# Performance work log

Measured on AMD Instinct MI355X. Metric: run time of the kernel, lower is better.

Reference implementation:

```python
import jax, jax.numpy as jnp
import numpy as np

N_NODES = 100000
N_EDGES = 1600000
IN_C, HID_C, OUT_C = 128, 64, 32


def gcn_conv(x, src, dst, dinv, W, b):
    # GCNConv: h = x W; out[i] = sum_{j->i} norm_ji * h[j] + b
    h = x @ W                                   # [N, C_out]
    norm = dinv[src] * dinv[dst]                # [E_tot]
    msg = h[src] * norm[:, None]                # gather + scale
    out = jax.ops.segment_sum(msg, dst, num_segments=N_NODES)
    return out + b


def setup_inputs() -> dict:
    key = jax.random.key(0)
    k1, k2, k3, k4 = jax.random.split(key, 4)
    x = jax.random.normal(k1, (N_NODES, IN_C), dtype=jnp.float32)
    edge_index = jax.random.randint(k2, (2, N_EDGES), 0, N_NODES, dtype=jnp.int64)
    # Glorot-ish init for weights
    W1 = jax.random.normal(k3, (IN_C, HID_C), dtype=jnp.float32) * (1.0 / np.sqrt(IN_C))
    b1 = jnp.zeros((HID_C,), dtype=jnp.float32)
    W2 = jax.random.normal(k4, (HID_C, OUT_C), dtype=jnp.float32) * (1.0 / np.sqrt(HID_C))
    b2 = jnp.zeros((OUT_C,), dtype=jnp.float32)
    return {"x": x, "edge_index": edge_index, "W1": W1, "b1": b1, "W2": W2, "b2": b2}


def reference(x, edge_index, W1, b1, W2, b2):
    # Add self loops (GCNConv default), compute symmetric normalization once.
    loop = jnp.arange(N_NODES, dtype=edge_index.dtype)
    src = jnp.concatenate([edge_index[0], loop])   # [E + N]
    dst = jnp.concatenate([edge_index[1], loop])
    deg = jax.ops.segment_sum(jnp.ones_like(src, dtype=x.dtype), dst,
                              num_segments=N_NODES)
    dinv = jnp.where(deg > 0, jax.lax.rsqrt(jnp.maximum(deg, 1e-12)), 0.0)

    h = gcn_conv(x, src, dst, dinv, W1, b1)
    h = jax.nn.relu(h)
    # F.dropout with training=False (eval mode) is identity
    out = gcn_conv(h, src, dst, dinv, W2, b2)
    return out
```

## Files before the change

kernel.cpp:

```cpp
#include <hip/hip_runtime.h>

#define N_NODES 100000
#define N_EDGES 1600000
#define IN_C 128
#define HID_C 64
#define OUT_C 32

#define NBUCK 782
#define NBLK_B 256
#define CHUNK 6250
#define BSTRIDE 1024
#define MAXPT 12

#define GROWS 16
#define GEMM_BLKS 6250

typedef unsigned int uint;
typedef unsigned short ushort;

__device__ inline ushort f2bf(float f) {
    uint u = __float_as_uint(f);
    u += 0x7fff + ((u >> 16) & 1);
    return (ushort)(u >> 16);
}
__device__ inline float bf2f(ushort h) {
    return __uint_as_float(((uint)h) << 16);
}


__global__ __launch_bounds__(256) void k_bucket_count(const int* __restrict__ dst,
                                                      int* __restrict__ bcnt) {
    __shared__ int h[NBUCK];
    int t = threadIdx.x;
    for (int b = t; b < NBUCK; b += 256) h[b] = 0;
    __syncthreads();
    int base = blockIdx.x * CHUNK;
    int end = base + CHUNK;
    for (int i = base + t; i < end; i += 256) atomicAdd(&h[dst[i] >> 7], 1);
    __syncthreads();
    for (int b = t; b < NBUCK; b += 256) bcnt[blockIdx.x * BSTRIDE + b] = h[b];
}


__global__ __launch_bounds__(256) void k_col_scan(const int* __restrict__ bcnt,
                                                  int* __restrict__ off,
                                                  int* __restrict__ total) {
    __shared__ int ps[256];
    int t = threadIdx.x, b = blockIdx.x;
    int l = bcnt[t * BSTRIDE + b];
    ps[t] = l;
    __syncthreads();
    for (int o = 1; o < 256; o <<= 1) {
        int u = (t >= o) ? ps[t - o] : 0;
        __syncthreads();
        ps[t] += u;
        __syncthreads();
    }
    off[t * BSTRIDE + b] = ps[t] - l;
    if (t == 255) total[b] = ps[255];
}


__global__ __launch_bounds__(256) void k_bucket_scan(const int* __restrict__ total,
                                                     int* __restrict__ bucket_start,
                                                     int* __restrict__ row_start) {
    __shared__ int ps[256];
    int t = threadIdx.x;
    int v[4];
    int base = t * 4;
#pragma unroll
    for (int q = 0; q < 4; ++q) v[q] = (base + q < NBUCK) ? total[base + q] : 0;
    ps[t] = v[0] + v[1] + v[2] + v[3];
    __syncthreads();
    for (int o = 1; o < 256; o <<= 1) {
        int u = (t >= o) ? ps[t - o] : 0;
        __syncthreads();
        ps[t] += u;
        __syncthreads();
    }
    int run = (t > 0) ? ps[t - 1] : 0;
#pragma unroll
    for (int q = 0; q < 4; ++q) {
        if (base + q <= NBUCK) bucket_start[base + q] = run;
        run += v[q];
    }
    if (t == 0) row_start[N_NODES] = N_EDGES;
}


__global__ __launch_bounds__(256) void k_scatter_fat(const int* __restrict__ src,
                                                     const int* __restrict__ dst,
                                                     const int* __restrict__ bucket_start,
                                                     const int* __restrict__ off,
                                                     int* __restrict__ tmp,
                                                     const float* __restrict__ x,
                                                     const float* __restrict__ W1,
                                                     ushort* __restrict__ h1b) {
    __shared__ float smem[GROWS * IN_C];
    int t = threadIdx.x;
    if (blockIdx.x < NBLK_B) {
        int* cur = (int*)smem;
        for (int b = t; b < NBUCK; b += 256)
            cur[b] = bucket_start[b] + off[blockIdx.x * BSTRIDE + b];
        __syncthreads();
        int base = blockIdx.x * CHUNK;
        int end = base + CHUNK;
        for (int i = base + t; i < end; i += 256) {
            int s = src[i], d = dst[i];
            int b = d >> 7;
            int p = atomicAdd(&cur[b], 1);
            tmp[p] = (s << 7) | (d & 127);
        }
    } else {
        int rowbase = (blockIdx.x - NBLK_B) * GROWS;
#pragma unroll
        for (int q = 0; q < 8; ++q)
            smem[q * 256 + t] = x[rowbase * IN_C + q * 256 + t];
        __syncthreads();
        int wave = t >> 6, lane = t & 63;
        int rl0 = wave * 4;
        float a0 = 0.f, a1 = 0.f, a2 = 0.f, a3 = 0.f;
#pragma unroll 8
        for (int k = 0; k < IN_C; ++k) {
            float w = W1[k * HID_C + lane];
            a0 += smem[(rl0 + 0) * IN_C + k] * w;
            a1 += smem[(rl0 + 1) * IN_C + k] * w;
            a2 += smem[(rl0 + 2) * IN_C + k] * w;
            a3 += smem[(rl0 + 3) * IN_C + k] * w;
        }
        int row = rowbase + rl0;
        h1b[(row + 0) * HID_C + lane] = f2bf(a0);
        h1b[(row + 1) * HID_C + lane] = f2bf(a1);
        h1b[(row + 2) * HID_C + lane] = f2bf(a2);
        h1b[(row + 3) * HID_C + lane] = f2bf(a3);
    }
}


__global__ __launch_bounds__(256) void k_csr_build(const int* __restrict__ bucket_start,
                                                   const int* __restrict__ tmp,
                                                   int* __restrict__ row_start,
                                                   int* __restrict__ eidx,
                                                   float* __restrict__ dinv) {
    __shared__ int h[128];
    __shared__ int cur[128];
    int b = blockIdx.x, t = threadIdx.x;
    int e0 = bucket_start[b], e1 = bucket_start[b + 1];
    if (t < 128) h[t] = 0;
    int pk[MAXPT];
#pragma unroll
    for (int k = 0; k < MAXPT; ++k) {
        int i = e0 + k * 256 + t;
        pk[k] = (i < e1) ? tmp[i] : -1;
    }
    __syncthreads();
#pragma unroll
    for (int k = 0; k < MAXPT; ++k)
        if (pk[k] >= 0) atomicAdd(&h[pk[k] & 127], 1);
    for (int i = e0 + MAXPT * 256 + t; i < e1; i += 256)
        atomicAdd(&h[tmp[i] & 127], 1);
    __syncthreads();
    int d0 = (t < 128) ? h[t] : 0;
    for (int o = 1; o < 128; o <<= 1) {
        int u = (t >= o && t < 128) ? h[t - o] : 0;
        __syncthreads();
        if (t < 128) h[t] += u;
        __syncthreads();
    }
    int g = b * 128 + t;
    if (t < 128 && g < N_NODES) {
        int ex = h[t] - d0;
        row_start[g] = e0 + ex;
        cur[t]       = e0 + ex;
        dinv[g] = rsqrtf((float)(d0 + 1));
    }
    __syncthreads();
#pragma unroll
    for (int k = 0; k < MAXPT; ++k)
        if (pk[k] >= 0) {
            int p = atomicAdd(&cur[pk[k] & 127], 1);
            eidx[p] = pk[k] >> 7;
        }
    for (int i = e0 + MAXPT * 256 + t; i < e1; i += 256) {
        int v = tmp[i];
        int p = atomicAdd(&cur[v & 127], 1);
        eidx[p] = v >> 7;
    }
}


__global__ __launch_bounds__(256) void k_gather1f(const int* __restrict__ row_start,
                                                  const int* __restrict__ eidx,
                                                  const uint* __restrict__ h1u,
                                                  const float* __restrict__ dinv,
                                                  const float* __restrict__ b1,
                                                  const float* __restrict__ W2,
                                                  ushort* __restrict__ hs2b) {
    __shared__ float a1s[8][HID_C];
    __shared__ float W2s[HID_C * OUT_C];
    int t = threadIdx.x;
    for (int i = t; i < HID_C * OUT_C; i += 256) W2s[i] = W2[i];
    int sub = t & 31;
    int r = t >> 5;
    float2 bb = *(const float2*)&b1[sub * 2];

    for (int g = 0; g < 4; ++g) {
        int node = (blockIdx.x * 4 + g) * 8 + r;
        float dn = dinv[node];
        int rs = row_start[node];
        int re = row_start[node + 1];
        uint su = h1u[node * 32 + sub];
        float accx = dn * __uint_as_float(su << 16);
        float accy = dn * __uint_as_float(su & 0xffff0000u);
        int j = rs;
        for (; j + 7 < re; j += 8) {
            int s0 = eidx[j],     s1 = eidx[j + 1], s2 = eidx[j + 2], s3 = eidx[j + 3];
            int s4 = eidx[j + 4], s5 = eidx[j + 5], s6 = eidx[j + 6], s7 = eidx[j + 7];
            float g0 = dinv[s0], g1 = dinv[s1], g2 = dinv[s2], g3 = dinv[s3];
            float g4 = dinv[s4], g5 = dinv[s5], g6 = dinv[s6], g7 = dinv[s7];
            uint u0 = h1u[s0 * 32 + sub], u1 = h1u[s1 * 32 + sub];
            uint u2 = h1u[s2 * 32 + sub], u3 = h1u[s3 * 32 + sub];
            uint u4 = h1u[s4 * 32 + sub], u5 = h1u[s5 * 32 + sub];
            uint u6 = h1u[s6 * 32 + sub], u7 = h1u[s7 * 32 + sub];
            accx += g0 * __uint_as_float(u0 << 16) + g1 * __uint_as_float(u1 << 16)
                  + g2 * __uint_as_float(u2 << 16) + g3 * __uint_as_float(u3 << 16)
                  + g4 * __uint_as_float(u4 << 16) + g5 * __uint_as_float(u5 << 16)
                  + g6 * __uint_as_float(u6 << 16) + g7 * __uint_as_float(u7 << 16);
            accy += g0 * __uint_as_float(u0 & 0xffff0000u) + g1 * __uint_as_float(u1 & 0xffff0000u)
                  + g2 * __uint_as_float(u2 & 0xffff0000u) + g3 * __uint_as_float(u3 & 0xffff0000u)
                  + g4 * __uint_as_float(u4 & 0xffff0000u) + g5 * __uint_as_float(u5 & 0xffff0000u)
                  + g6 * __uint_as_float(u6 & 0xffff0000u) + g7 * __uint_as_float(u7 & 0xffff0000u);
        }
        for (; j + 3 < re; j += 4) {
            int s0 = eidx[j], s1 = eidx[j + 1], s2 = eidx[j + 2], s3 = eidx[j + 3];
            float g0 = dinv[s0], g1 = dinv[s1], g2 = dinv[s2], g3 = dinv[s3];
            uint u0 = h1u[s0 * 32 + sub], u1 = h1u[s1 * 32 + sub];
            uint u2 = h1u[s2 * 32 + sub], u3 = h1u[s3 * 32 + sub];
            accx += g0 * __uint_as_float(u0 << 16) + g1 * __uint_as_float(u1 << 16)
                  + g2 * __uint_as_float(u2 << 16) + g3 * __uint_as_float(u3 << 16);
            accy += g0 * __uint_as_float(u0 & 0xffff0000u) + g1 * __uint_as_float(u1 & 0xffff0000u)
                  + g2 * __uint_as_float(u2 & 0xffff0000u) + g3 * __uint_as_float(u3 & 0xffff0000u);
        }
        for (; j < re; ++j) {
            int s = eidx[j];
            float gg = dinv[s];
            uint u = h1u[s * 32 + sub];
            accx += gg * __uint_as_float(u << 16);
            accy += gg * __uint_as_float(u & 0xffff0000u);
        }
        __syncthreads();
        a1s[r][sub * 2 + 0] = fmaxf(dn * accx + bb.x, 0.f);
        a1s[r][sub * 2 + 1] = fmaxf(dn * accy + bb.y, 0.f);
        __syncthreads();

        float sum = 0.f;
#pragma unroll 8
        for (int k = 0; k < HID_C; ++k)
            sum += a1s[r][k] * W2s[k * OUT_C + sub];
        hs2b[node * OUT_C + sub] = f2bf(dn * sum);
    }
}


__global__ __launch_bounds__(256) void k_gather2(const int* __restrict__ row_start,
                                                 const int* __restrict__ eidx,
                                                 const ushort* __restrict__ hs2b,
                                                 const float* __restrict__ dinv,
                                                 const float* __restrict__ b2,
                                                 float* __restrict__ out) {
    int t = threadIdx.x;
    int sub = t & 31;
    int node = blockIdx.x * 8 + (t >> 5);

    float dn = dinv[node];
    int rs = row_start[node];
    int re = row_start[node + 1];
    float acc = bf2f(hs2b[node * OUT_C + sub]);
    int j = rs;
    for (; j + 7 < re; j += 8) {
        int s0 = eidx[j],     s1 = eidx[j + 1], s2 = eidx[j + 2], s3 = eidx[j + 3];
        int s4 = eidx[j + 4], s5 = eidx[j + 5], s6 = eidx[j + 6], s7 = eidx[j + 7];
        float v0 = bf2f(hs2b[s0 * OUT_C + sub]);
        float v1 = bf2f(hs2b[s1 * OUT_C + sub]);
        float v2 = bf2f(hs2b[s2 * OUT_C + sub]);
        float v3 = bf2f(hs2b[s3 * OUT_C + sub]);
        float v4 = bf2f(hs2b[s4 * OUT_C + sub]);
        float v5 = bf2f(hs2b[s5 * OUT_C + sub]);
        float v6 = bf2f(hs2b[s6 * OUT_C + sub]);
        float v7 = bf2f(hs2b[s7 * OUT_C + sub]);
        acc += ((v0 + v1) + (v2 + v3)) + ((v4 + v5) + (v6 + v7));
    }
    for (; j + 3 < re; j += 4) {
        int s0 = eidx[j], s1 = eidx[j + 1], s2 = eidx[j + 2], s3 = eidx[j + 3];
        float v0 = bf2f(hs2b[s0 * OUT_C + sub]);
        float v1 = bf2f(hs2b[s1 * OUT_C + sub]);
        float v2 = bf2f(hs2b[s2 * OUT_C + sub]);
        float v3 = bf2f(hs2b[s3 * OUT_C + sub]);
        acc += (v0 + v1) + (v2 + v3);
    }
    for (; j < re; ++j) acc += bf2f(hs2b[eidx[j] * OUT_C + sub]);

    out[node * OUT_C + sub] = dn * acc + b2[sub];
}

extern "C" void kernel_launch(void* const* d_in, const int* in_sizes, int n_in,
                              void* d_out, int out_size, void* d_ws, size_t ws_size,
                              hipStream_t stream) {
    const float* x  = (const float*)d_in[0];
    const int* ei   = (const int*)d_in[1];
    const float* W1 = (const float*)d_in[2];
    const float* b1 = (const float*)d_in[3];
    const float* W2 = (const float*)d_in[4];
    const float* b2 = (const float*)d_in[5];
    float* out = (float*)d_out;

    const int* src = ei;
    const int* dst = ei + N_EDGES;

    char* ws = (char*)d_ws;
    int*    row_start    = (int*)(ws + 0);
    float*  dinv         = (float*)(ws + 400128);
    int*    bucket_start = (int*)(ws + 800256);
    int*    total        = (int*)(ws + 804352);
    int*    bcnt         = (int*)(ws + 808448);
    int*    off          = (int*)(ws + 1857024);
    int*    eidx         = (int*)(ws + 2905600);
    int*    tmp          = (int*)(ws + 9305600);
    ushort* h1b          = (ushort*)(ws + 15705600);
    ushort* hs2b         = (ushort*)(ws + 28505600);

    k_bucket_count<<<NBLK_B, 256, 0, stream>>>(dst, bcnt);
    k_col_scan<<<NBUCK, 256, 0, stream>>>(bcnt, off, total);
    k_bucket_scan<<<1, 256, 0, stream>>>(total, bucket_start, row_start);

    k_scatter_fat<<<NBLK_B + GEMM_BLKS, 256, 0, stream>>>(src, dst, bucket_start, off,
                                                          tmp, x, W1, h1b);
    k_csr_build<<<NBUCK, 256, 0, stream>>>(bucket_start, tmp, row_start, eidx, dinv);

    k_gather1f<<<N_NODES / 32, 256, 0, stream>>>(row_start, eidx, (const uint*)h1b,
                                                 dinv, b1, W2, hs2b);
    k_gather2<<<N_NODES / 8, 256, 0, stream>>>(row_start, eidx, hs2b, dinv, b2, out);
}
```

Baseline: 162.6 us.

## Use bf16 MFMA for first GEMM and prescale h1 by dinv in CSR build

```diff
diff --git a/kernel.cpp b/kernel.cpp
--- a/kernel.cpp
+++ b/kernel.cpp
@@ -12,11 +12,12 @@
 #define BSTRIDE 1024
 #define MAXPT 12
 
-#define GROWS 16
-#define GEMM_BLKS 6250
+#define MF_BLKS 1563
 
 typedef unsigned int uint;
 typedef unsigned short ushort;
+typedef __attribute__((ext_vector_type(8))) short bf16x8;
+typedef __attribute__((ext_vector_type(4))) float f32x4;
 
 __device__ inline ushort f2bf(float f) {
     uint u = __float_as_uint(f);
@@ -96,10 +97,10 @@
                                                      const float* __restrict__ x,
                                                      const float* __restrict__ W1,
                                                      ushort* __restrict__ h1b) {
-    __shared__ float smem[GROWS * IN_C];
+    __shared__ uint smu[4096];
     int t = threadIdx.x;
     if (blockIdx.x < NBLK_B) {
-        int* cur = (int*)smem;
+        int* cur = (int*)smu;
         for (int b = t; b < NBUCK; b += 256)
             cur[b] = bucket_start[b] + off[blockIdx.x * BSTRIDE + b];
         __syncthreads();
@@ -112,27 +113,58 @@
             tmp[p] = (s << 7) | (d & 127);
         }
     } else {
-        int rowbase = (blockIdx.x - NBLK_B) * GROWS;
-#pragma unroll
-        for (int q = 0; q < 8; ++q)
-            smem[q * 256 + t] = x[rowbase * IN_C + q * 256 + t];
+        int g = blockIdx.x - NBLK_B;
+#pragma unroll
+        for (int i = 0; i < 16; ++i) {
+            int lin = i * 256 + t;
+            int frag = lin >> 8;
+            int lane_ = (lin >> 2) & 63;
+            int dw = lin & 3;
+            int k = ((frag >> 2) << 5) + ((lane_ >> 4) << 3) + dw * 2;
+            int c = ((frag & 3) << 4) + (lane_ & 15);
+            smu[lin] = ((uint)f2bf(W1[(k + 1) * HID_C + c]) << 16) | f2bf(W1[k * HID_C + c]);
+        }
         __syncthreads();
         int wave = t >> 6, lane = t & 63;
-        int rl0 = wave * 4;
-        float a0 = 0.f, a1 = 0.f, a2 = 0.f, a3 = 0.f;
-#pragma unroll 8
-        for (int k = 0; k < IN_C; ++k) {
-            float w = W1[k * HID_C + lane];
-            a0 += smem[(rl0 + 0) * IN_C + k] * w;
-            a1 += smem[(rl0 + 1) * IN_C + k] * w;
-            a2 += smem[(rl0 + 2) * IN_C + k] * w;
-            a3 += smem[(rl0 + 3) * IN_C + k] * w;
-        }
-        int row = rowbase + rl0;
-        h1b[(row + 0) * HID_C + lane] = f2bf(a0);
-        h1b[(row + 1) * HID_C + lane] = f2bf(a1);
-        h1b[(row + 2) * HID_C + lane] = f2bf(a2);
-        h1b[(row + 3) * HID_C + lane] = f2bf(a3);
+        int row0 = g * 64 + wave * 16;
+        bf16x8 bfr[4][4];
+#pragma unroll
+        for (int kt = 0; kt < 4; ++kt)
+#pragma unroll
+            for (int ct = 0; ct < 4; ++ct)
+                bfr[kt][ct] = *(bf16x8*)&smu[((kt * 4 + ct) * 64 + lane) * 4];
+        int arow = row0 + (lane & 15);
+        if (arow > N_NODES - 1) arow = N_NODES - 1;
+        int kbase = (lane >> 4) * 8;
+        f32x4 acc0 = {0.f, 0.f, 0.f, 0.f}, acc1 = {0.f, 0.f, 0.f, 0.f};
+        f32x4 acc2 = {0.f, 0.f, 0.f, 0.f}, acc3 = {0.f, 0.f, 0.f, 0.f};
+#pragma unroll
+        for (int kt = 0; kt < 4; ++kt) {
+            const float* xp = &x[arow * IN_C + kt * 32 + kbase];
+            float4 u0 = *(const float4*)xp;
+            float4 u1 = *(const float4*)(xp + 4);
+            union { uint u[4]; bf16x8 v; } A;
+            A.u[0] = ((uint)f2bf(u0.y) << 16) | f2bf(u0.x);
+            A.u[1] = ((uint)f2bf(u0.w) << 16) | f2bf(u0.z);
+            A.u[2] = ((uint)f2bf(u1.y) << 16) | f2bf(u1.x);
+            A.u[3] = ((uint)f2bf(u1.w) << 16) | f2bf(u1.z);
+            acc0 = __builtin_amdgcn_mfma_f32_16x16x32_bf16(A.v, bfr[kt][0], acc0, 0, 0, 0);
+            acc1 = __builtin_amdgcn_mfma_f32_16x16x32_bf16(A.v, bfr[kt][1], acc1, 0, 0, 0);
+            acc2 = __builtin_amdgcn_mfma_f32_16x16x32_bf16(A.v, bfr[kt][2], acc2, 0, 0, 0);
+            acc3 = __builtin_amdgcn_mfma_f32_16x16x32_bf16(A.v, bfr[kt][3], acc3, 0, 0, 0);
+        }
+        int rbase = row0 + ((lane >> 4) << 2);
+        int cb = lane & 15;
+#pragma unroll
+        for (int r = 0; r < 4; ++r) {
+            int row = rbase + r;
+            if (row < N_NODES) {
+                h1b[row * HID_C + cb]      = f2bf(acc0[r]);
+                h1b[row * HID_C + 16 + cb] = f2bf(acc1[r]);
+                h1b[row * HID_C + 32 + cb] = f2bf(acc2[r]);
+                h1b[row * HID_C + 48 + cb] = f2bf(acc3[r]);
+            }
+        }
     }
 }
 
@@ -141,9 +173,11 @@
                                                    const int* __restrict__ tmp,
                                                    int* __restrict__ row_start,
                                                    int* __restrict__ eidx,
-                                                   float* __restrict__ dinv) {
+                                                   float* __restrict__ dinv,
+                                                   uint* __restrict__ h1u) {
     __shared__ int h[128];
     __shared__ int cur[128];
+    __shared__ float dl[128];
     int b = blockIdx.x, t = threadIdx.x;
     int e0 = bucket_start[b], e1 = bucket_start[b + 1];
     if (t < 128) h[t] = 0;
@@ -172,7 +206,9 @@
         int ex = h[t] - d0;
         row_start[g] = e0 + ex;
         cur[t]       = e0 + ex;
-        dinv[g] = rsqrtf((float)(d0 + 1));
+        float dv = rsqrtf((float)(d0 + 1));
+        dinv[g] = dv;
+        dl[t] = dv;
     }
     __syncthreads();
 #pragma unroll
@@ -185,6 +221,18 @@
         int v = tmp[i];
         int p = atomicAdd(&cur[v & 127], 1);
         eidx[p] = v >> 7;
+    }
+    int bu = b * 128 * (HID_C / 2);
+    for (int i = t; i < 128 * (HID_C / 2); i += 256) {
+        int rl = i >> 5;
+        int gg = b * 128 + rl;
+        if (gg < N_NODES) {
+            float dv = dl[rl];
+            uint v = h1u[bu + i];
+            float lo = __uint_as_float(v << 16) * dv;
+            float hi = __uint_as_float(v & 0xffff0000u) * dv;
+            h1u[bu + i] = ((uint)f2bf(hi) << 16) | f2bf(lo);
+        }
     }
 }
 
@@ -210,43 +258,38 @@
         int rs = row_start[node];
         int re = row_start[node + 1];
         uint su = h1u[node * 32 + sub];
-        float accx = dn * __uint_as_float(su << 16);
-        float accy = dn * __uint_as_float(su & 0xffff0000u);
+        float accx = __uint_as_float(su << 16);
+        float accy = __uint_as_float(su & 0xffff0000u);
         int j = rs;
         for (; j + 7 < re; j += 8) {
             int s0 = eidx[j],     s1 = eidx[j + 1], s2 = eidx[j + 2], s3 = eidx[j + 3];
             int s4 = eidx[j + 4], s5 = eidx[j + 5], s6 = eidx[j + 6], s7 = eidx[j + 7];
-            float g0 = dinv[s0], g1 = dinv[s1], g2 = dinv[s2], g3 = dinv[s3];
-            float g4 = dinv[s4], g5 = dinv[s5], g6 = dinv[s6], g7 = dinv[s7];
             uint u0 = h1u[s0 * 32 + sub], u1 = h1u[s1 * 32 + sub];
             uint u2 = h1u[s2 * 32 + sub], u3 = h1u[s3 * 32 + sub];
             uint u4 = h1u[s4 * 32 + sub], u5 = h1u[s5 * 32 + sub];
             uint u6 = h1u[s6 * 32 + sub], u7 = h1u[s7 * 32 + sub];
-            accx += g0 * __uint_as_float(u0 << 16) + g1 * __uint_as_float(u1 << 16)
-                  + g2 * __uint_as_float(u2 << 16) + g3 * __uint_as_float(u3 << 16)
-                  + g4 * __uint_as_float(u4 << 16) + g5 * __uint_as_float(u5 << 16)
-                  + g6 * __uint_as_float(u6 << 16) + g7 * __uint_as_float(u7 << 16);
-            accy += g0 * __uint_as_float(u0 & 0xffff0000u) + g1 * __uint_as_float(u1 & 0xffff0000u)
-                  + g2 * __uint_as_float(u2 & 0xffff0000u) + g3 * __uint_as_float(u3 & 0xffff0000u)
-                  + g4 * __uint_as_float(u4 & 0xffff0000u) + g5 * __uint_as_float(u5 & 0xffff0000u)
-                  + g6 * __uint_as_float(u6 & 0xffff0000u) + g7 * __uint_as_float(u7 & 0xffff0000u);
+            accx += (__uint_as_float(u0 << 16) + __uint_as_float(u1 << 16))
+                  + (__uint_as_float(u2 << 16) + __uint_as_float(u3 << 16))
+                  + (__uint_as_float(u4 << 16) + __uint_as_float(u5 << 16))
+                  + (__uint_as_float(u6 << 16) + __uint_as_float(u7 << 16));
+            accy += (__uint_as_float(u0 & 0xffff0000u) + __uint_as_float(u1 & 0xffff0000u))
+                  + (__uint_as_float(u2 & 0xffff0000u) + __uint_as_float(u3 & 0xffff0000u))
+                  + (__uint_as_float(u4 & 0xffff0000u) + __uint_as_float(u5 & 0xffff0000u))
+                  + (__uint_as_float(u6 & 0xffff0000u) + __uint_as_float(u7 & 0xffff0000u));
         }
         for (; j + 3 < re; j += 4) {
             int s0 = eidx[j], s1 = eidx[j + 1], s2 = eidx[j + 2], s3 = eidx[j + 3];
-            float g0 = dinv[s0], g1 = dinv[s1], g2 = dinv[s2], g3 = dinv[s3];
             uint u0 = h1u[s0 * 32 + sub], u1 = h1u[s1 * 32 + sub];
             uint u2 = h1u[s2 * 32 + sub], u3 = h1u[s3 * 32 + sub];
-            accx += g0 * __uint_as_float(u0 << 16) + g1 * __uint_as_float(u1 << 16)
-                  + g2 * __uint_as_float(u2 << 16) + g3 * __uint_as_float(u3 << 16);
-            accy += g0 * __uint_as_float(u0 & 0xffff0000u) + g1 * __uint_as_float(u1 & 0xffff0000u)
-                  + g2 * __uint_as_float(u2 & 0xffff0000u) + g3 * __uint_as_float(u3 & 0xffff0000u);
+            accx += (__uint_as_float(u0 << 16) + __uint_as_float(u1 << 16))
+                  + (__uint_as_float(u2 << 16) + __uint_as_float(u3 << 16));
+            accy += (__uint_as_float(u0 & 0xffff0000u) + __uint_as_float(u1 & 0xffff0000u))
+                  + (__uint_as_float(u2 & 0xffff0000u) + __uint_as_float(u3 & 0xffff0000u));
         }
         for (; j < re; ++j) {
-            int s = eidx[j];
-            float gg = dinv[s];
-            uint u = h1u[s * 32 + sub];
-            accx += gg * __uint_as_float(u << 16);
-            accy += gg * __uint_as_float(u & 0xffff0000u);
+            uint u = h1u[eidx[j] * 32 + sub];
+            accx += __uint_as_float(u << 16);
+            accy += __uint_as_float(u & 0xffff0000u);
         }
         __syncthreads();
         a1s[r][sub * 2 + 0] = fmaxf(dn * accx + bb.x, 0.f);
@@ -333,9 +376,10 @@
     k_col_scan<<<NBUCK, 256, 0, stream>>>(bcnt, off, total);
     k_bucket_scan<<<1, 256, 0, stream>>>(total, bucket_start, row_start);
 
-    k_scatter_fat<<<NBLK_B + GEMM_BLKS, 256, 0, stream>>>(src, dst, bucket_start, off,
-                                                          tmp, x, W1, h1b);
-    k_csr_build<<<NBUCK, 256, 0, stream>>>(bucket_start, tmp, row_start, eidx, dinv);
+    k_scatter_fat<<<NBLK_B + MF_BLKS, 256, 0, stream>>>(src, dst, bucket_start, off,
+                                                        tmp, x, W1, h1b);
+    k_csr_build<<<NBUCK, 256, 0, stream>>>(bucket_start, tmp, row_start, eidx, dinv,
+                                           (uint*)h1b);
 
     k_gather1f<<<N_NODES / 32, 256, 0, stream>>>(row_start, eidx, (const uint*)h1b,
                                                  dinv, b1, W2, hs2b);
```

Result: faster. 148.2 us (-8.8%).
